# Kernel optimization log

Measured on AMD Instinct MI355X. Metric: run time of the kernel, lower is better.

## Reference

```python
import jax, jax.numpy as jnp
import numpy as np

N = 50000
E = 800000
C_IN, C_HID, C_OUT = 512, 128, 2
HEADS2 = 3
NEG_SLOPE = 0.2


def gat_conv(x, src, dst, W, att_src, att_dst, bias, heads, ch, concat):
    """PyG GATConv (eval mode) on pre-augmented (self-loop included) edge lists.
    x: [N, F_in], W: [F_in, heads*ch], att_*: [heads, ch], bias: [heads*ch] or [ch].
    """
    n = x.shape[0]
    h = (x @ W).reshape(n, heads, ch)                 # [N, H, C]
    a_src = (h * att_src).sum(-1)                     # [N, H]
    a_dst = (h * att_dst).sum(-1)                     # [N, H]
    e = jax.nn.leaky_relu(a_src[src] + a_dst[dst], NEG_SLOPE)  # [E', H]
    # segment softmax over edges sharing a destination node
    m = jax.ops.segment_max(e, dst, num_segments=n)
    m = jnp.where(jnp.isfinite(m), m, 0.0)
    ex = jnp.exp(e - m[dst])
    denom = jax.ops.segment_sum(ex, dst, num_segments=n)
    alpha = ex / (denom[dst] + 1e-16)                 # [E', H]
    out = jax.ops.segment_sum(h[src] * alpha[:, :, None], dst, num_segments=n)  # [N, H, C]
    out = out.reshape(n, heads * ch) if concat else out.mean(axis=1)
    return out + bias


def setup_inputs() -> dict:
    key = jax.random.key(0)
    ks = jax.random.split(key, 12)
    x = jax.random.normal(ks[0], (N, C_IN), dtype=jnp.float32)
    edge_index = jax.random.randint(ks[1], (2, E), 0, N, dtype=jnp.int64)
    s1 = 1.0 / np.sqrt(C_IN)
    s2 = 1.0 / np.sqrt(C_HID)
    return {
        "x": x,
        "edge_index": edge_index,
        "W1": jax.random.normal(ks[2], (C_IN, C_HID), dtype=jnp.float32) * s1,
        "att_src1": jax.random.normal(ks[3], (1, C_HID), dtype=jnp.float32) * s2,
        "att_dst1": jax.random.normal(ks[4], (1, C_HID), dtype=jnp.float32) * s2,
        "bias1": jnp.zeros((C_HID,), dtype=jnp.float32),
        "W2": jax.random.normal(ks[5], (C_HID, HEADS2 * C_OUT), dtype=jnp.float32) * s2,
        "att_src2": jax.random.normal(ks[6], (HEADS2, C_OUT), dtype=jnp.float32) * 0.5,
        "att_dst2": jax.random.normal(ks[7], (HEADS2, C_OUT), dtype=jnp.float32) * 0.5,
        "bias2": jnp.zeros((C_OUT,), dtype=jnp.float32),
    }


def reference(x, edge_index, W1, att_src1, att_dst1, bias1, W2, att_src2, att_dst2, bias2):
    n = x.shape[0]
    loop = jnp.arange(n, dtype=edge_index.dtype)
    src = jnp.concatenate([edge_index[0], loop])      # PyG add_self_loops=True
    dst = jnp.concatenate([edge_index[1], loop])
    h = gat_conv(x, src, dst, W1, att_src1, att_dst1, bias1, 1, C_HID, True)
    h = jax.nn.relu(h)                                # Dropout is identity in eval
    out = gat_conv(h, src, dst, W2, att_src2, att_dst2, bias2, HEADS2, C_OUT, False)
    return out
```

## Files before the change

### kernel.cpp

```cpp
#include <hip/hip_runtime.h>

#define N_NODES 50000
#define N_EDGES 800000
#define E_TOT   850000
#define C_IN    512
#define C_HID   128
#define NEG     0.2f

typedef _Float16 f16x8 __attribute__((ext_vector_type(8)));
typedef __attribute__((ext_vector_type(4))) float f32x4;

__device__ __forceinline__ float leaky(float x) { return x > 0.f ? x : NEG * x; }

union U32H2 { unsigned u; _Float16 h[2]; float f; };

__device__ __forceinline__ unsigned short f2h(float f) {
  U32H2 c; c.h[0] = (_Float16)f; return (unsigned short)(c.u & 0xffff);
}

__device__ __forceinline__ unsigned pk2h(float a, float b) {
  union { __fp16 v __attribute__((ext_vector_type(2))); unsigned u; } c;
  c.v = __builtin_amdgcn_cvt_pkrtz(a, b);
  return c.u;
}

__global__ __launch_bounds__(256) void prep_v_kernel(const float* __restrict__ W1,
    const float* __restrict__ as1, const float* __restrict__ ad1,
    float* __restrict__ v1s, float* __restrict__ v1d) {
  const int wv = threadIdx.x >> 6, lane = threadIdx.x & 63;
  const int k = blockIdx.x * 4 + wv;
  if (k >= C_IN) return;
  float2 w = *(const float2*)(W1 + (size_t)k * C_HID + 2 * lane);
  float2 a = *(const float2*)(as1 + 2 * lane);
  float2 d = *(const float2*)(ad1 + 2 * lane);
  float s = w.x * a.x + w.y * a.y;
  float t = w.x * d.x + w.y * d.y;
#pragma unroll
  for (int m = 32; m >= 1; m >>= 1) {
    s += __shfl_xor(s, m, 64);
    t += __shfl_xor(t, m, 64);
  }
  if (lane == 0) { v1s[k] = s; v1d[k] = t; }
}

__global__ __launch_bounds__(256) void prep_w_kernel(const float* __restrict__ W1,
    unsigned short* __restrict__ Wh, unsigned short* __restrict__ Wl) {
  int t = blockIdx.x * 256 + threadIdx.x;
  int c = t >> 5, k0 = (t & 31) * 16;
  if (c >= C_HID) return;
#pragma unroll
  for (int i = 0; i < 16; i++) {
    float w = W1[(size_t)(k0 + i) * C_HID + c];
    _Float16 hi = (_Float16)w;
    _Float16 lo = (_Float16)(w - (float)hi);
    U32H2 ch; ch.h[0] = hi;
    U32H2 cl; cl.h[0] = lo;
    Wh[(size_t)c * C_IN + k0 + i] = (unsigned short)(ch.u & 0xffff);
    Wl[(size_t)c * C_IN + k0 + i] = (unsigned short)(cl.u & 0xffff);
  }
}

__global__ __launch_bounds__(256) void lin1_kernel(const float* __restrict__ x,
    const unsigned short* __restrict__ Wh, const unsigned short* __restrict__ Wl,
    const float* __restrict__ v1s, const float* __restrict__ v1d,
    unsigned short* __restrict__ h1u, float* __restrict__ a_src, float* __restrict__ a_dst) {
  __shared__ __attribute__((aligned(16))) unsigned short As[64][40];
  __shared__ __attribute__((aligned(16))) unsigned short Bh[128][40];
  __shared__ __attribute__((aligned(16))) unsigned short Bl[128][40];

  const int tid  = threadIdx.x;
  const int lane = tid & 63, wv = tid >> 6;
  const int m0   = blockIdx.x * 64;

  const int arow = tid >> 2, kseg = (tid & 3) * 8;
  int grow = m0 + arow;
  if (grow >= N_NODES) grow = N_NODES - 1;
  const float* xrow = x + (size_t)grow * C_IN + kseg;

  const int bcol = tid >> 1, bhalf = tid & 1;
  const unsigned short* whp = Wh + (size_t)bcol * C_IN + bhalf * 16;
  const unsigned short* wlp = Wl + (size_t)bcol * C_IN + bhalf * 16;

  f32x4 acc[8];
#pragma unroll
  for (int b = 0; b < 8; b++) acc[b] = (f32x4)0.f;
  float ps = 0.f, pd = 0.f;

  const int q = lane >> 4, l15 = lane & 15;

  for (int k0 = 0; k0 < C_IN; k0 += 32) {
    float4 xa = *(const float4*)(xrow + k0);
    float4 xb = *(const float4*)(xrow + k0 + 4);
    float4 vsa = *(const float4*)(v1s + k0 + kseg);
    float4 vsb = *(const float4*)(v1s + k0 + kseg + 4);
    float4 vda = *(const float4*)(v1d + k0 + kseg);
    float4 vdb = *(const float4*)(v1d + k0 + kseg + 4);
    ps += xa.x * vsa.x + xa.y * vsa.y + xa.z * vsa.z + xa.w * vsa.w
        + xb.x * vsb.x + xb.y * vsb.y + xb.z * vsb.z + xb.w * vsb.w;
    pd += xa.x * vda.x + xa.y * vda.y + xa.z * vda.z + xa.w * vda.w
        + xb.x * vdb.x + xb.y * vdb.y + xb.z * vdb.z + xb.w * vdb.w;
    *(uint4*)&As[arow][kseg] = make_uint4(pk2h(xa.x, xa.y), pk2h(xa.z, xa.w),
                                          pk2h(xb.x, xb.y), pk2h(xb.z, xb.w));
    {
      const int4* sh = (const int4*)(whp + k0);
      const int4* sl = (const int4*)(wlp + k0);
      int4* dh = (int4*)&Bh[bcol][bhalf * 16];
      int4* dl = (int4*)&Bl[bcol][bhalf * 16];
      dh[0] = sh[0]; dh[1] = sh[1];
      dl[0] = sl[0]; dl[1] = sl[1];
    }
    __syncthreads();

    f16x8 a0 = *(const f16x8*)&As[wv * 16 + l15][q * 8];
#pragma unroll
    for (int t = 0; t < 8; t++) {
      f16x8 bh = *(const f16x8*)&Bh[t * 16 + l15][q * 8];
      f16x8 bl = *(const f16x8*)&Bl[t * 16 + l15][q * 8];
      acc[t] = __builtin_amdgcn_mfma_f32_16x16x32_f16(a0, bh, acc[t], 0, 0, 0);
      acc[t] = __builtin_amdgcn_mfma_f32_16x16x32_f16(a0, bl, acc[t], 0, 0, 0);
    }
    __syncthreads();
  }

  ps += __shfl_xor(ps, 1, 64); ps += __shfl_xor(ps, 2, 64);
  pd += __shfl_xor(pd, 1, 64); pd += __shfl_xor(pd, 2, 64);
  if ((tid & 3) == 0) {
    int row = m0 + arow;
    if (row < N_NODES) { a_src[row] = ps; a_dst[row] = pd; }
  }

  {
    int rbase = m0 + wv * 16 + q * 4;
#pragma unroll
    for (int t = 0; t < 8; t++) {
#pragma unroll
      for (int ri = 0; ri < 4; ri++) {
        int row = rbase + ri;
        if (row < N_NODES)
          h1u[(size_t)row * C_HID + t * 16 + l15] = f2h(acc[t][ri]);
      }
    }
  }
}

__global__ void deg_kernel(const int* __restrict__ ei, int* __restrict__ deg) {
  int e = blockIdx.x * blockDim.x + threadIdx.x;
  if (e >= N_EDGES) return;
  atomicAdd(&deg[ei[N_EDGES + e]], 1);
}

__global__ __launch_bounds__(1024) void scan_kernel(const int* __restrict__ deg,
                                                    int* __restrict__ rowptr,
                                                    int* __restrict__ cursor) {
  __shared__ int wsum[16];
  const int tid = threadIdx.x, lane = tid & 63, wv = tid >> 6;
  int carry = 0;
  for (int base = 0; base < N_NODES; base += 8192) {
    int i0 = base + tid * 8;
    int v[8];
    if (i0 + 8 <= N_NODES) {
      int4 va = *(const int4*)(deg + i0);
      int4 vb = *(const int4*)(deg + i0 + 4);
      v[0]=va.x+1; v[1]=va.y+1; v[2]=va.z+1; v[3]=va.w+1;
      v[4]=vb.x+1; v[5]=vb.y+1; v[6]=vb.z+1; v[7]=vb.w+1;
    } else {
#pragma unroll
      for (int i = 0; i < 8; i++) v[i] = (i0 + i < N_NODES) ? deg[i0 + i] + 1 : 0;
    }
    int tsum = 0;
#pragma unroll
    for (int i = 0; i < 8; i++) tsum += v[i];
    int sc = tsum;
#pragma unroll
    for (int off = 1; off < 64; off <<= 1) {
      int t = __shfl_up(sc, off, 64);
      if (lane >= off) sc += t;
    }
    if (lane == 63) wsum[wv] = sc;
    __syncthreads();
    if (wv == 0 && lane < 16) {
      int s = wsum[lane];
#pragma unroll
      for (int off = 1; off < 16; off <<= 1) {
        int t = __shfl_up(s, off, 64);
        if (lane >= off) s += t;
      }
      wsum[lane] = s;
    }
    __syncthreads();
    int ex = carry + (wv ? wsum[wv - 1] : 0) + sc - tsum;
#pragma unroll
    for (int i = 0; i < 8; i++) {
      if (i0 + i < N_NODES) { rowptr[i0 + i] = ex; cursor[i0 + i] = ex; }
      ex += v[i];
    }
    carry += wsum[15];
    __syncthreads();
  }
  if (tid == 0) rowptr[N_NODES] = carry;
}

__global__ void bucket_kernel(const int* __restrict__ ei, int* __restrict__ cursor,
                              const float* __restrict__ a_src, const float* __restrict__ a_dst,
                              int2* __restrict__ esw) {
  int e = blockIdx.x * blockDim.x + threadIdx.x;
  if (e >= E_TOT) return;
  int src, dst;
  if (e < N_EDGES) { src = ei[e]; dst = ei[N_EDGES + e]; }
  else             { src = dst = e - N_EDGES; }
  float w = __expf(leaky(a_src[src] + a_dst[dst]));
  int slot = atomicAdd(&cursor[dst], 1);
  U32H2 c; c.f = w;
  esw[slot] = make_int2(src, (int)c.u);
}

__global__ __launch_bounds__(256) void agg1_kernel(const unsigned short* __restrict__ h1u,
    const int2* __restrict__ esw, const int* __restrict__ rowptr,
    const float* __restrict__ bias1, const float* __restrict__ W2,
    const float* __restrict__ as2w, const float* __restrict__ ad2w,
    float* __restrict__ h2, float* __restrict__ as2, float* __restrict__ ad2) {
  const int wv = threadIdx.x >> 6, lane = threadIdx.x & 63;
  const int q = lane >> 4, r = lane & 15;
  const int n = blockIdx.x * 4 + wv;
  if (n >= N_NODES) return;
  const int start = rowptr[n], end = rowptr[n + 1];

  float acc[8];
#pragma unroll
  for (int i = 0; i < 8; i++) acc[i] = 0.f;
  float wsum = 0.f;

  const unsigned short* hbase = h1u + r * 8;

  for (int base = start; base < end; base += 64) {
    int idx = base + lane;
    int sreg = 0; float wreg = 0.f;
    if (idx < end) {
      int2 sv = esw[idx];
      sreg = sv.x;
      U32H2 c; c.u = (unsigned)sv.y;
      wreg = c.f;
    }
    wsum += wreg;
    const int cnt = min(64, end - base);
    const int nit = (cnt + 7) >> 3;
    for (int i = 0; i < nit; i++) {
      int e0 = 8 * i + q, e1 = 8 * i + 4 + q;
      int   s0 = __shfl(sreg, e0, 64);
      int   s1 = __shfl(sreg, e1, 64);
      float w0 = __shfl(wreg, e0, 64);
      float w1 = __shfl(wreg, e1, 64);
      uint4 g0 = *(const uint4*)(hbase + (size_t)s0 * C_HID);
      uint4 g1 = *(const uint4*)(hbase + (size_t)s1 * C_HID);
      U32H2 c0, c1, c2, c3;
      c0.u = g0.x; c1.u = g0.y; c2.u = g0.z; c3.u = g0.w;
      acc[0] = fmaf(w0, (float)c0.h[0], acc[0]); acc[1] = fmaf(w0, (float)c0.h[1], acc[1]);
      acc[2] = fmaf(w0, (float)c1.h[0], acc[2]); acc[3] = fmaf(w0, (float)c1.h[1], acc[3]);
      acc[4] = fmaf(w0, (float)c2.h[0], acc[4]); acc[5] = fmaf(w0, (float)c2.h[1], acc[5]);
      acc[6] = fmaf(w0, (float)c3.h[0], acc[6]); acc[7] = fmaf(w0, (float)c3.h[1], acc[7]);
      c0.u = g1.x; c1.u = g1.y; c2.u = g1.z; c3.u = g1.w;
      acc[0] = fmaf(w1, (float)c0.h[0], acc[0]); acc[1] = fmaf(w1, (float)c0.h[1], acc[1]);
      acc[2] = fmaf(w1, (float)c1.h[0], acc[2]); acc[3] = fmaf(w1, (float)c1.h[1], acc[3]);
      acc[4] = fmaf(w1, (float)c2.h[0], acc[4]); acc[5] = fmaf(w1, (float)c2.h[1], acc[5]);
      acc[6] = fmaf(w1, (float)c3.h[0], acc[6]); acc[7] = fmaf(w1, (float)c3.h[1], acc[7]);
    }
  }

#pragma unroll
  for (int i = 0; i < 8; i++) {
    acc[i] += __shfl_xor(acc[i], 16, 64);
    acc[i] += __shfl_xor(acc[i], 32, 64);
  }
#pragma unroll
  for (int m = 32; m >= 1; m >>= 1) wsum += __shfl_xor(wsum, m, 64);
  const float inv = 1.f / wsum;

  float4 ba = *(const float4*)(bias1 + r * 8);
  float4 bb = *(const float4*)(bias1 + r * 8 + 4);
  float u[8] = {fmaxf(acc[0] * inv + ba.x, 0.f), fmaxf(acc[1] * inv + ba.y, 0.f),
                fmaxf(acc[2] * inv + ba.z, 0.f), fmaxf(acc[3] * inv + ba.w, 0.f),
                fmaxf(acc[4] * inv + bb.x, 0.f), fmaxf(acc[5] * inv + bb.y, 0.f),
                fmaxf(acc[6] * inv + bb.z, 0.f), fmaxf(acc[7] * inv + bb.w, 0.f)};
  float p[6] = {0, 0, 0, 0, 0, 0};
#pragma unroll
  for (int i = 0; i < 8; i++) {
    const float* w2r = W2 + (size_t)(r * 8 + i) * 6;
#pragma unroll
    for (int o = 0; o < 6; o++) p[o] = fmaf(u[i], w2r[o], p[o]);
  }
#pragma unroll
  for (int o = 0; o < 6; o++) {
#pragma unroll
    for (int msk = 8; msk >= 1; msk >>= 1) p[o] += __shfl_xor(p[o], msk, 64);
  }

  if (lane == 0) {
#pragma unroll
    for (int o = 0; o < 6; o++) h2[(size_t)n * 8 + o] = p[o];
#pragma unroll
    for (int h = 0; h < 3; h++) {
      as2[n * 4 + h] = p[2 * h] * as2w[2 * h] + p[2 * h + 1] * as2w[2 * h + 1];
      ad2[n * 4 + h] = p[2 * h] * ad2w[2 * h] + p[2 * h + 1] * ad2w[2 * h + 1];
    }
  }
}

__global__ __launch_bounds__(256) void agg2_kernel(const float* __restrict__ h2,
    const float* __restrict__ as2, const float* __restrict__ ad2,
    const int* __restrict__ rowptr, const int2* __restrict__ esw,
    const float* __restrict__ bias2, float* __restrict__ out) {
  const int wv = threadIdx.x >> 6, lane = threadIdx.x & 63;
  const int q = lane >> 4, r = lane & 15;
  const int n = blockIdx.x * 16 + wv * 4 + q;
  if (n >= N_NODES) return;
  const int start = rowptr[n], end = rowptr[n + 1];
  const float4 adv = *(const float4*)(ad2 + (size_t)n * 4);

  float d0 = 0.f, d1 = 0.f, d2 = 0.f;
  float a0 = 0.f, a1 = 0.f, a2 = 0.f, a3 = 0.f, a4 = 0.f, a5 = 0.f;
  for (int j = start + r; j < end; j += 16) {
    int s = esw[j].x;
    float4 asv = *(const float4*)(as2 + (size_t)s * 4);
    float4 hlo = *(const float4*)(h2 + (size_t)s * 8);
    float2 hhi = *(const float2*)(h2 + (size_t)s * 8 + 4);
    float e0 = __expf(leaky(asv.x + adv.x));
    float e1 = __expf(leaky(asv.y + adv.y));
    float e2 = __expf(leaky(asv.z + adv.z));
    d0 += e0; d1 += e1; d2 += e2;
    a0 += e0 * hlo.x; a1 += e0 * hlo.y;
    a2 += e1 * hlo.z; a3 += e1 * hlo.w;
    a4 += e2 * hhi.x; a5 += e2 * hhi.y;
  }
#pragma unroll
  for (int m = 8; m >= 1; m >>= 1) {
    d0 += __shfl_xor(d0, m, 64); d1 += __shfl_xor(d1, m, 64); d2 += __shfl_xor(d2, m, 64);
    a0 += __shfl_xor(a0, m, 64); a1 += __shfl_xor(a1, m, 64); a2 += __shfl_xor(a2, m, 64);
    a3 += __shfl_xor(a3, m, 64); a4 += __shfl_xor(a4, m, 64); a5 += __shfl_xor(a5, m, 64);
  }
  if (r == 0) {
    float o0 = (a0 / d0 + a2 / d1 + a4 / d2) * (1.f / 3.f) + bias2[0];
    float o1 = (a1 / d0 + a3 / d1 + a5 / d2) * (1.f / 3.f) + bias2[1];
    *(float2*)(out + (size_t)n * 2) = make_float2(o0, o1);
  }
}

extern "C" void kernel_launch(void* const* d_in, const int* in_sizes, int n_in,
                              void* d_out, int out_size, void* d_ws, size_t ws_size,
                              hipStream_t stream) {
  const float* x        = (const float*)d_in[0];
  const int*   ei       = (const int*)d_in[1];
  const float* W1       = (const float*)d_in[2];
  const float* att_src1 = (const float*)d_in[3];
  const float* att_dst1 = (const float*)d_in[4];
  const float* bias1    = (const float*)d_in[5];
  const float* W2       = (const float*)d_in[6];
  const float* att_src2 = (const float*)d_in[7];
  const float* att_dst2 = (const float*)d_in[8];
  const float* bias2    = (const float*)d_in[9];
  float* out = (float*)d_out;

  char* w = (char*)d_ws;
  auto alloc = [&](size_t bytes) {
    char* p = w;
    w += (bytes + 255) & ~(size_t)255;
    return p;
  };
  unsigned short* h1u    = (unsigned short*)alloc((size_t)N_NODES * C_HID * 2);
  unsigned short* W1Th   = (unsigned short*)alloc((size_t)C_IN * C_HID * 2);
  unsigned short* W1Tl   = (unsigned short*)alloc((size_t)C_IN * C_HID * 2);
  float*          v1s    = (float*)alloc((size_t)C_IN * 4);
  float*          v1d    = (float*)alloc((size_t)C_IN * 4);
  float*          a_src1 = (float*)alloc((size_t)N_NODES * 4);
  float*          a_dst1 = (float*)alloc((size_t)N_NODES * 4);
  int*            deg    = (int*)alloc((size_t)N_NODES * 4);
  int*            rowptr = (int*)alloc((size_t)(N_NODES + 4) * 4);
  int*            cursor = (int*)alloc((size_t)N_NODES * 4);
  int2*           esw    = (int2*)alloc((size_t)E_TOT * 8);
  float*          h2     = (float*)alloc((size_t)N_NODES * 8 * 4);
  float*          as2    = (float*)alloc((size_t)N_NODES * 4 * 4);
  float*          ad2    = (float*)alloc((size_t)N_NODES * 4 * 4);

  (void)hipMemsetAsync(deg, 0, (size_t)N_NODES * 4, stream);

  prep_v_kernel<<<C_IN / 4, 256, 0, stream>>>(W1, att_src1, att_dst1, v1s, v1d);
  prep_w_kernel<<<16, 256, 0, stream>>>(W1, W1Th, W1Tl);
  deg_kernel<<<(N_EDGES + 255) / 256, 256, 0, stream>>>(ei, deg);
  scan_kernel<<<1, 1024, 0, stream>>>(deg, rowptr, cursor);
  lin1_kernel<<<(N_NODES + 63) / 64, 256, 0, stream>>>(x, W1Th, W1Tl, v1s, v1d,
                                                       h1u, a_src1, a_dst1);
  bucket_kernel<<<(E_TOT + 255) / 256, 256, 0, stream>>>(ei, cursor, a_src1, a_dst1, esw);
  agg1_kernel<<<(N_NODES + 3) / 4, 256, 0, stream>>>(h1u, esw, rowptr, bias1, W2,
                                                     att_src2, att_dst2, h2, as2, ad2);
  agg2_kernel<<<(N_NODES + 15) / 16, 256, 0, stream>>>(h2, as2, ad2, rowptr, esw, bias2, out);
}
```

Measured before the change: 363.1 us.

## Pre-swizzle W1 into MFMA fragment layout and load B directly from global

The weight prep kernel now writes the split-fp16 W1 (hi and lo parts) in the exact per-lane MFMA B-fragment order, so lin1 loads B operands straight from global and cache with one 16-byte load per fragment instead of staging them through shared memory. The warp mapping changes so each wave owns 32 output columns across all 64 rows, reusing each B fragment over four row tiles. The x row loads are software-prefetched one k-block ahead. This removes the B shared-memory traffic and halves LDS use, at the cost of more global or L2 reads of W per block and more A-fragment LDS reads per wave.

Measured after the change: 354.1 us. 1.03x faster.

```diff
diff --git a/kernel.cpp b/kernel.cpp
--- a/kernel.cpp
+++ b/kernel.cpp
@@ -13,6 +13,7 @@
 __device__ __forceinline__ float leaky(float x) { return x > 0.f ? x : NEG * x; }
 
 union U32H2 { unsigned u; _Float16 h[2]; float f; };
+union BFrag { uint4 u; f16x8 h; };
 
 __device__ __forceinline__ unsigned short f2h(float f) {
   U32H2 c; c.h[0] = (_Float16)f; return (unsigned short)(c.u & 0xffff);
@@ -44,29 +45,34 @@
 }
 
 __global__ __launch_bounds__(256) void prep_w_kernel(const float* __restrict__ W1,
-    unsigned short* __restrict__ Wh, unsigned short* __restrict__ Wl) {
+    unsigned short* __restrict__ Wswz) {
   int t = blockIdx.x * 256 + threadIdx.x;
-  int c = t >> 5, k0 = (t & 31) * 16;
+  int c = t >> 6, kc = t & 63;
   if (c >= C_HID) return;
-#pragma unroll
-  for (int i = 0; i < 16; i++) {
-    float w = W1[(size_t)(k0 + i) * C_HID + c];
+  int kblk = kc >> 2, q = kc & 3;
+  int ct = c >> 4, l15 = c & 15;
+  int lane = q * 16 + l15;
+  unsigned short hb[8], lb[8];
+#pragma unroll
+  for (int i = 0; i < 8; i++) {
+    float w = W1[(size_t)(kc * 8 + i) * C_HID + c];
     _Float16 hi = (_Float16)w;
     _Float16 lo = (_Float16)(w - (float)hi);
     U32H2 ch; ch.h[0] = hi;
     U32H2 cl; cl.h[0] = lo;
-    Wh[(size_t)c * C_IN + k0 + i] = (unsigned short)(ch.u & 0xffff);
-    Wl[(size_t)c * C_IN + k0 + i] = (unsigned short)(cl.u & 0xffff);
-  }
+    hb[i] = (unsigned short)(ch.u & 0xffff);
+    lb[i] = (unsigned short)(cl.u & 0xffff);
+  }
+  size_t chunk0 = ((size_t)(kblk * 8 + ct) * 2) * 512;
+  *(uint4*)&Wswz[chunk0 + (size_t)lane * 8]       = *(uint4*)hb;
+  *(uint4*)&Wswz[chunk0 + 512 + (size_t)lane * 8] = *(uint4*)lb;
 }
 
 __global__ __launch_bounds__(256) void lin1_kernel(const float* __restrict__ x,
-    const unsigned short* __restrict__ Wh, const unsigned short* __restrict__ Wl,
+    const unsigned short* __restrict__ Wswz,
     const float* __restrict__ v1s, const float* __restrict__ v1d,
     unsigned short* __restrict__ h1u, float* __restrict__ a_src, float* __restrict__ a_dst) {
   __shared__ __attribute__((aligned(16))) unsigned short As[64][40];
-  __shared__ __attribute__((aligned(16))) unsigned short Bh[128][40];
-  __shared__ __attribute__((aligned(16))) unsigned short Bl[128][40];
 
   const int tid  = threadIdx.x;
   const int lane = tid & 63, wv = tid >> 6;
@@ -77,20 +83,18 @@
   if (grow >= N_NODES) grow = N_NODES - 1;
   const float* xrow = x + (size_t)grow * C_IN + kseg;
 
-  const int bcol = tid >> 1, bhalf = tid & 1;
-  const unsigned short* whp = Wh + (size_t)bcol * C_IN + bhalf * 16;
-  const unsigned short* wlp = Wl + (size_t)bcol * C_IN + bhalf * 16;
-
-  f32x4 acc[8];
-#pragma unroll
-  for (int b = 0; b < 8; b++) acc[b] = (f32x4)0.f;
+  f32x4 acc[4][2];
+#pragma unroll
+  for (int rt = 0; rt < 4; rt++) { acc[rt][0] = (f32x4)0.f; acc[rt][1] = (f32x4)0.f; }
   float ps = 0.f, pd = 0.f;
 
   const int q = lane >> 4, l15 = lane & 15;
 
-  for (int k0 = 0; k0 < C_IN; k0 += 32) {
-    float4 xa = *(const float4*)(xrow + k0);
-    float4 xb = *(const float4*)(xrow + k0 + 4);
+  float4 xa = *(const float4*)(xrow);
+  float4 xb = *(const float4*)(xrow + 4);
+
+  for (int kblk = 0; kblk < 16; kblk++) {
+    const int k0 = kblk * 32;
     float4 vsa = *(const float4*)(v1s + k0 + kseg);
     float4 vsb = *(const float4*)(v1s + k0 + kseg + 4);
     float4 vda = *(const float4*)(v1d + k0 + kseg);
@@ -99,27 +103,32 @@
         + xb.x * vsb.x + xb.y * vsb.y + xb.z * vsb.z + xb.w * vsb.w;
     pd += xa.x * vda.x + xa.y * vda.y + xa.z * vda.z + xa.w * vda.w
         + xb.x * vdb.x + xb.y * vdb.y + xb.z * vdb.z + xb.w * vdb.w;
-    *(uint4*)&As[arow][kseg] = make_uint4(pk2h(xa.x, xa.y), pk2h(xa.z, xa.w),
-                                          pk2h(xb.x, xb.y), pk2h(xb.z, xb.w));
-    {
-      const int4* sh = (const int4*)(whp + k0);
-      const int4* sl = (const int4*)(wlp + k0);
-      int4* dh = (int4*)&Bh[bcol][bhalf * 16];
-      int4* dl = (int4*)&Bl[bcol][bhalf * 16];
-      dh[0] = sh[0]; dh[1] = sh[1];
-      dl[0] = sl[0]; dl[1] = sl[1];
-    }
+    uint4 pk = make_uint4(pk2h(xa.x, xa.y), pk2h(xa.z, xa.w),
+                          pk2h(xb.x, xb.y), pk2h(xb.z, xb.w));
+
     __syncthreads();
-
-    f16x8 a0 = *(const f16x8*)&As[wv * 16 + l15][q * 8];
-#pragma unroll
-    for (int t = 0; t < 8; t++) {
-      f16x8 bh = *(const f16x8*)&Bh[t * 16 + l15][q * 8];
-      f16x8 bl = *(const f16x8*)&Bl[t * 16 + l15][q * 8];
-      acc[t] = __builtin_amdgcn_mfma_f32_16x16x32_f16(a0, bh, acc[t], 0, 0, 0);
-      acc[t] = __builtin_amdgcn_mfma_f32_16x16x32_f16(a0, bl, acc[t], 0, 0, 0);
+    *(uint4*)&As[arow][kseg] = pk;
+    if (kblk < 15) {
+      xa = *(const float4*)(xrow + k0 + 32);
+      xb = *(const float4*)(xrow + k0 + 36);
     }
     __syncthreads();
+
+    const unsigned short* bp = Wswz + ((size_t)(kblk * 8 + wv * 2) * 2) * 512 + (size_t)lane * 8;
+    BFrag b00, b01, b10, b11;
+    b00.u = *(const uint4*)(bp);
+    b01.u = *(const uint4*)(bp + 512);
+    b10.u = *(const uint4*)(bp + 1024);
+    b11.u = *(const uint4*)(bp + 1536);
+
+#pragma unroll
+    for (int rt = 0; rt < 4; rt++) {
+      f16x8 af = *(const f16x8*)&As[rt * 16 + l15][q * 8];
+      acc[rt][0] = __builtin_amdgcn_mfma_f32_16x16x32_f16(af, b00.h, acc[rt][0], 0, 0, 0);
+      acc[rt][0] = __builtin_amdgcn_mfma_f32_16x16x32_f16(af, b01.h, acc[rt][0], 0, 0, 0);
+      acc[rt][1] = __builtin_amdgcn_mfma_f32_16x16x32_f16(af, b10.h, acc[rt][1], 0, 0, 0);
+      acc[rt][1] = __builtin_amdgcn_mfma_f32_16x16x32_f16(af, b11.h, acc[rt][1], 0, 0, 0);
+    }
   }
 
   ps += __shfl_xor(ps, 1, 64); ps += __shfl_xor(ps, 2, 64);
@@ -129,15 +138,17 @@
     if (row < N_NODES) { a_src[row] = ps; a_dst[row] = pd; }
   }
 
-  {
-    int rbase = m0 + wv * 16 + q * 4;
-#pragma unroll
-    for (int t = 0; t < 8; t++) {
+#pragma unroll
+  for (int rt = 0; rt < 4; rt++) {
+    int rbase = m0 + rt * 16 + q * 4;
+#pragma unroll
+    for (int ct = 0; ct < 2; ct++) {
+      int col = wv * 32 + ct * 16 + l15;
 #pragma unroll
       for (int ri = 0; ri < 4; ri++) {
         int row = rbase + ri;
         if (row < N_NODES)
-          h1u[(size_t)row * C_HID + t * 16 + l15] = f2h(acc[t][ri]);
+          h1u[(size_t)row * C_HID + col] = f2h(acc[rt][ct][ri]);
       }
     }
   }
@@ -366,8 +377,7 @@
     return p;
   };
   unsigned short* h1u    = (unsigned short*)alloc((size_t)N_NODES * C_HID * 2);
-  unsigned short* W1Th   = (unsigned short*)alloc((size_t)C_IN * C_HID * 2);
-  unsigned short* W1Tl   = (unsigned short*)alloc((size_t)C_IN * C_HID * 2);
+  unsigned short* Wswz   = (unsigned short*)alloc((size_t)C_IN * C_HID * 2 * 2);
   float*          v1s    = (float*)alloc((size_t)C_IN * 4);
   float*          v1d    = (float*)alloc((size_t)C_IN * 4);
   float*          a_src1 = (float*)alloc((size_t)N_NODES * 4);
@@ -383,10 +393,10 @@
   (void)hipMemsetAsync(deg, 0, (size_t)N_NODES * 4, stream);
 
   prep_v_kernel<<<C_IN / 4, 256, 0, stream>>>(W1, att_src1, att_dst1, v1s, v1d);
-  prep_w_kernel<<<16, 256, 0, stream>>>(W1, W1Th, W1Tl);
+  prep_w_kernel<<<32, 256, 0, stream>>>(W1, Wswz);
   deg_kernel<<<(N_EDGES + 255) / 256, 256, 0, stream>>>(ei, deg);
   scan_kernel<<<1, 1024, 0, stream>>>(deg, rowptr, cursor);
-  lin1_kernel<<<(N_NODES + 63) / 64, 256, 0, stream>>>(x, W1Th, W1Tl, v1s, v1d,
+  lin1_kernel<<<(N_NODES + 63) / 64, 256, 0, stream>>>(x, Wswz, v1s, v1d,
                                                        h1u, a_src1, a_dst1);
   bucket_kernel<<<(E_TOT + 255) / 256, 256, 0, stream>>>(ei, cursor, a_src1, a_dst1, esw);
   agg1_kernel<<<(N_NODES + 3) / 4, 256, 0, stream>>>(h1u, esw, rowptr, bias1, W2,
```
